# Performance work log

Measured on AMD Instinct MI355X. Metric: run time of the kernel, lower is better.

The kernel has to match this reference:

```python
import jax, jax.numpy as jnp
import numpy as np
import math

D_MODEL = 1024
NUM_HEADS = 16
MAX_LEN = 2048
D_HEAD = D_MODEL // NUM_HEADS
BATCH = 2
SEQ = 2048


def setup_inputs() -> dict:
    root = jax.random.key(0)
    ks = jax.random.split(root, 10)
    s = 1.0 / math.sqrt(D_MODEL)
    return {
        "query": jax.random.normal(ks[0], (BATCH, SEQ, D_MODEL), jnp.float32),
        "key": jax.random.normal(ks[1], (BATCH, SEQ, D_MODEL), jnp.float32),
        "value": jax.random.normal(ks[2], (BATCH, SEQ, D_MODEL), jnp.float32),
        "Wq": jax.random.normal(ks[3], (D_MODEL, D_MODEL), jnp.float32) * s,
        "bq": jax.random.normal(ks[4], (D_MODEL,), jnp.float32) * s,
        "Wk": jax.random.normal(ks[5], (D_MODEL, D_MODEL), jnp.float32) * s,
        "bk": jax.random.normal(ks[6], (D_MODEL,), jnp.float32) * s,
        "Wv": jax.random.normal(ks[7], (D_MODEL, D_MODEL), jnp.float32) * s,
        "bv": jax.random.normal(ks[8], (D_MODEL,), jnp.float32) * s,
        "Er": jax.random.normal(ks[9], (MAX_LEN, D_HEAD), jnp.float32),
    }


def _skew(QEr):
    # QEr: [B, H, S, S] -> pad one zero column on the left, reshape, drop first row
    B, H, R, C = QEr.shape
    padded = jnp.pad(QEr, ((0, 0), (0, 0), (0, 0), (1, 0)))  # [B,H,R,C+1]
    reshaped = padded.reshape(B, H, C + 1, R)
    return reshaped[:, :, 1:, :]  # [B,H,R,C] == Srel


def reference(query, key, value, Wq, bq, Wk, bk, Wv, bv, Er):
    B, S, D = query.shape
    H, dh = NUM_HEADS, D_HEAD
    # nn.Linear: x @ W.T + b
    q = (jnp.einsum("bsd,ed->bse", query, Wq) + bq).reshape(B, S, H, dh).transpose(0, 2, 1, 3)  # [B,H,S,dh]
    k = (jnp.einsum("bsd,ed->bse", key, Wk) + bk).reshape(B, S, H, dh).transpose(0, 2, 1, 3)
    v = (jnp.einsum("bsd,ed->bse", value, Wv) + bv).reshape(B, S, H, dh).transpose(0, 2, 1, 3)
    start = MAX_LEN - S
    Er_s = Er[start:, :]  # [S, dh]
    QEr = jnp.einsum("bhsd,ld->bhsl", q, Er_s)  # [B,H,S,S]
    Srel = _skew(QEr)
    QK = jnp.einsum("bhsd,bhtd->bhst", q, k)
    attn = (QK + Srel) / math.sqrt(dh)
    causal = jnp.tril(jnp.ones((S, S), dtype=bool))
    attn = jnp.where(causal[None, None], attn, -jnp.inf)
    attn = jax.nn.softmax(attn, axis=-1)
    out = jnp.einsum("bhst,bhtd->bhsd", attn, v)  # [B,H,S,dh]
    out = out.transpose(0, 2, 1, 3).reshape(B, S, D)
    return out  # dropout is identity in eval mode
```

## Files before the change

kernel.cpp:

```cpp
#include <hip/hip_runtime.h>
#include <hip/hip_bf16.h>

typedef __attribute__((ext_vector_type(8))) short bf16x8;
typedef __attribute__((ext_vector_type(4))) float f32x4;

#define DEVI __device__ __forceinline__
#define AS1 __attribute__((address_space(1)))
#define AS3 __attribute__((address_space(3)))

constexpr int SEQ_   = 2048;
constexpr int HEADS  = 16;
constexpr int DHEAD  = 64;
constexpr int DMODEL = 1024;

DEVI unsigned short f2bf(float x) {
  __hip_bfloat16 h = __float2bfloat16(x);
  return __builtin_bit_cast(unsigned short, h);
}

DEVI f32x4 MFMA(bf16x8 a, bf16x8 b, f32x4 c) {
  return __builtin_amdgcn_mfma_f32_16x16x32_bf16(a, b, c, 0, 0, 0);
}

DEVI unsigned int cvtpk(float lo, float hi) {
  unsigned int u;
  asm("v_cvt_pk_bf16_f32 %0, %1, %2" : "=v"(u) : "v"(lo), "v"(hi));
  return u;
}

DEVI float exp2v(float x) {
  float y;
  asm("v_exp_f32 %0, %1" : "=v"(y) : "v"(x));
  return y;
}

__global__ void conv_all_kernel(const float* q, const float* k, const float* v,
                                const float* Wq, const float* Wk, const float* Wv,
                                const float* Er,
                                unsigned short* Xq, unsigned short* Xk,
                                unsigned short* Xv,
                                unsigned short* Wqb, unsigned short* Wkb,
                                unsigned short* Wvb, unsigned short* Erb) {
  const int y = blockIdx.y;
  const int i = (blockIdx.x * 256 + threadIdx.x) * 8;
  const float* s;
  unsigned short* d;
  int off = i;
  if (y < 3) {
    if (i >= 2 * SEQ_ * DMODEL) return;
    s = (y == 0) ? q : (y == 1) ? k : v;
    d = (y == 0) ? Xq : (y == 1) ? Xk : Xv;
  } else {
    constexpr int NW = DMODEL * DMODEL;
    if (i >= 3 * NW + SEQ_ * DHEAD) return;
    if (i < NW)          { s = Wq; d = Wqb; }
    else if (i < 2 * NW) { s = Wk; d = Wkb; off = i - NW; }
    else if (i < 3 * NW) { s = Wv; d = Wvb; off = i - 2 * NW; }
    else                 { s = Er; d = Erb; off = i - 3 * NW; }
  }
  const float4* p = (const float4*)(s + off);
  float4 v0 = p[0], v1 = p[1];
  union { unsigned short u[8]; bf16x8 v; } t;
  t.u[0] = f2bf(v0.x); t.u[1] = f2bf(v0.y); t.u[2] = f2bf(v0.z); t.u[3] = f2bf(v0.w);
  t.u[4] = f2bf(v1.x); t.u[5] = f2bf(v1.y); t.u[6] = f2bf(v1.z); t.u[7] = f2bf(v1.w);
  *(bf16x8*)(d + off) = t.v;
}

__global__ __launch_bounds__(256) void proj3_kernel(
    const unsigned short* __restrict__ X0, const unsigned short* __restrict__ X1,
    const unsigned short* __restrict__ X2,
    const unsigned short* __restrict__ W0, const unsigned short* __restrict__ W1,
    const unsigned short* __restrict__ W2,
    const float* __restrict__ bi0, const float* __restrict__ bi1,
    const float* __restrict__ bi2,
    unsigned short* __restrict__ o0, unsigned short* __restrict__ o1,
    unsigned short* __restrict__ o2) {
  const int z = blockIdx.z;
  const unsigned short* X = (z == 0) ? X0 : (z == 1) ? X1 : X2;
  const unsigned short* W = (z == 0) ? W0 : (z == 1) ? W1 : W2;
  const float* bias        = (z == 0) ? bi0 : (z == 1) ? bi1 : bi2;
  unsigned short* out      = (z == 0) ? o0 : (z == 1) ? o1 : o2;

  __shared__ unsigned short Abuf[2][128 * 32];
  __shared__ unsigned short Bbuf[2][128 * 32];
  const int tid  = threadIdx.x;
  const int lane = tid & 63, wv = tid >> 6;
  const int q = lane >> 4, r = lane & 15;
  const int wrow = wv >> 1, wcol = wv & 1;
  const int rowA0 = blockIdx.x * 128, colB0 = blockIdx.y * 128;

  const char* Ag = (const char*)(X + (size_t)rowA0 * DMODEL);
  const char* Bg = (const char*)(W + (size_t)colB0 * DMODEL);

  f32x4 acc[4][4] = {};

  auto stage = [&](int ks, int buf) {
    const int koff = ks * 64;
#pragma unroll
    for (int i = 0; i < 2; ++i) {
      const int b   = (i * 256 + tid) * 16;
      const int row = b >> 6, col = b & 63;
      __builtin_amdgcn_global_load_lds(
          (const AS1 void*)(Ag + (size_t)row * (DMODEL * 2) + koff + col),
          (AS3 void*)((char*)&Abuf[buf][0] + i * 4096 + wv * 1024),
          16, 0, 0);
      __builtin_amdgcn_global_load_lds(
          (const AS1 void*)(Bg + (size_t)row * (DMODEL * 2) + koff + col),
          (AS3 void*)((char*)&Bbuf[buf][0] + i * 4096 + wv * 1024),
          16, 0, 0);
    }
  };

  stage(0, 0);
  for (int ks = 0; ks < 32; ++ks) {
    __syncthreads();
    if (ks + 1 < 32) stage(ks + 1, (ks + 1) & 1);
    const unsigned short* A  = &Abuf[ks & 1][0];
    const unsigned short* Bt = &Bbuf[ks & 1][0];
    bf16x8 af[4], bfr[4];
#pragma unroll
    for (int t = 0; t < 4; ++t) {
      af[t]  = *(const bf16x8*)(A  + (wrow * 64 + t * 16 + r) * 32 + q * 8);
      bfr[t] = *(const bf16x8*)(Bt + (wcol * 64 + t * 16 + r) * 32 + q * 8);
    }
#pragma unroll
    for (int m = 0; m < 4; ++m)
#pragma unroll
      for (int n = 0; n < 4; ++n)
        acc[m][n] = MFMA(af[m], bfr[n], acc[m][n]);
  }

#pragma unroll
  for (int m = 0; m < 4; ++m) {
#pragma unroll
    for (int n = 0; n < 4; ++n) {
      const int e  = colB0 + wcol * 64 + n * 16 + r;
      const float bv = bias[e];
      const int h = e >> 6, dd = e & 63;
      const int nrow0 = rowA0 + wrow * 64 + m * 16 + q * 4;
      const int bb = nrow0 >> 11, ss0 = nrow0 & 2047;
      const size_t bh = (size_t)(bb * HEADS + h);
      if (z == 0) {
#pragma unroll
        for (int j = 0; j < 4; ++j)
          out[(bh * SEQ_ + (ss0 + j)) * DHEAD + dd] =
              f2bf((acc[m][n][j] + bv) * 0.1803368801111244f);
      } else if (z == 1) {
#pragma unroll
        for (int j = 0; j < 4; ++j) {
          const int s = ss0 + j;
          const size_t off = (bh * 64 + (size_t)(s >> 5)) * 2048
                           + (size_t)(((dd >> 5) * 2 + ((s >> 4) & 1)) * 512)
                           + (size_t)(((((dd & 31) >> 3) << 4) + (s & 15)) * 8)
                           + (dd & 7);
          out[off] = f2bf(acc[m][n][j] + bv);
        }
      } else {
#pragma unroll
        for (int j = 0; j < 4; ++j) {
          const int s = ss0 + j;
          const int tile64 = s >> 6, t = s & 63;
          const int tp = 4 * (t & 15) + (t >> 4);
          const int tc = tp >> 5, u = tp & 31;
          const int ln = ((u >> 3) << 4) | (dd & 15);
          const size_t off = (bh * 32 + (size_t)tile64) * 4096
                           + (size_t)(tc * 2048 + (dd >> 4) * 512 + ln * 8 + (u & 7));
          out[off] = f2bf(acc[m][n][j] + bv);
        }
      }
    }
  }
}

struct ErSet { bf16x8 e[8]; };

__global__ __launch_bounds__(256, 2) void attn_kernel(
    const unsigned short* __restrict__ qb, const unsigned short* __restrict__ kt,
    const unsigned short* __restrict__ vt, const unsigned short* __restrict__ Er,
    float* __restrict__ out, float* __restrict__ pO1, float* __restrict__ pL) {
  __shared__ unsigned short k_lds[3][4096];
  __shared__ unsigned short v_lds[3][4096];
  __shared__ unsigned short p_lds[4][32][68];

  const int tid  = threadIdx.x;
  const int lane = tid & 63, wv = tid >> 6;
  const int q = lane >> 4, r = lane & 15;

  const int lid = blockIdx.x;
  const int xcd = lid & 7, idx = lid >> 3;
  const int bh  = (xcd << 2) | (idx & 3);
  const int jb  = idx >> 2;
  const int p = jb >> 1, role = jb & 1;
  const int bb = bh >> 4, hh = bh & 15;

  const unsigned short* qbh = qb + (size_t)bh * SEQ_ * DHEAD;
  const char* ktb = (const char*)(kt + (size_t)bh * 64 * 2048);
  const char* vtb = (const char*)(vt + (size_t)bh * 32 * 4096);
  const f32x4 zero4 = {0.f, 0.f, 0.f, 0.f};

  const char* sgbase = (wv < 2) ? ktb : vtb;
  char* sdst0 = (char*)((wv < 2) ? &k_lds[0][0] : &v_lds[0][0]);
  const int shalf = (wv & 1) * 4096;
  const int soff  = lane * 16;

  auto stageKV = [&](int it, int buf) {
    const char* src = sgbase + (size_t)it * 8192 + shalf + soff;
    char* dst = sdst0 + buf * 8192 + shalf;
#pragma unroll
    for (int c = 0; c < 4; ++c)
      __builtin_amdgcn_global_load_lds((const AS1 void*)(src + c * 1024),
                                       (AS3 void*)(dst + c * 1024), 16, 0, 0);
  };

  auto run_strip = [&](int T, int it0, int it1, float* po, float* pl) {
    const int s0 = T * 128 + wv * 32;
    __syncthreads();
    stageKV(it0, 0);

    bf16x8 qf[2][2];
#pragma unroll
    for (int rt = 0; rt < 2; ++rt) {
      qf[rt][0] = *(const bf16x8*)(qbh + (size_t)(s0 + rt * 16 + r) * DHEAD + q * 8);
      qf[rt][1] = *(const bf16x8*)(qbh + (size_t)(s0 + rt * 16 + r) * DHEAD + 32 + q * 8);
    }

    f32x4 qer[2][6];
    {
      const int lb0 = 2016 + it0 * 64 - s0;
#pragma unroll
      for (int m = 0; m < 2; ++m) {
        int l = lb0 + m * 16 + r; l = l < 2047 ? l : 2047;
        bf16x8 e0 = *(const bf16x8*)(Er + (size_t)l * DHEAD + q * 8);
        bf16x8 e1 = *(const bf16x8*)(Er + (size_t)l * DHEAD + 32 + q * 8);
#pragma unroll
        for (int rt = 0; rt < 2; ++rt)
          qer[rt][m] = MFMA(qf[rt][1], e1, MFMA(qf[rt][0], e0, zero4));
      }
    }

    auto loadE = [&](ErSet& es, int it) {
      const int lb = 2016 + it * 64 - s0;
#pragma unroll
      for (int mi = 0; mi < 4; ++mi) {
        int l = lb + 32 + mi * 16 + r;
        l = l < 2047 ? l : 2047;
        es.e[mi * 2 + 0] = *(const bf16x8*)(Er + (size_t)l * DHEAD + q * 8);
        es.e[mi * 2 + 1] = *(const bf16x8*)(Er + (size_t)l * DHEAD + 32 + q * 8);
      }
    };

    f32x4 oacc[2][4] = {};
    float lpart[2][4] = {};

    auto body = [&](int it, int cur, const ErSet& es) {
      const int t0 = it * 64;
      if (t0 > s0 + 31) return;
      const unsigned short* KL = &k_lds[cur][0];
      const unsigned short* VL = &v_lds[cur][0];

      bf16x8 kf[4][2];
#pragma unroll
      for (int ct = 0; ct < 4; ++ct)
#pragma unroll
        for (int kc = 0; kc < 2; ++kc)
          kf[ct][kc] = *(const bf16x8*)(KL + (ct >> 1) * 2048 + (kc * 2 + (ct & 1)) * 512 + lane * 8);

      f32x4 s4[2][4];
      __builtin_amdgcn_s_setprio(1);
#pragma unroll
      for (int rt = 0; rt < 2; ++rt)
#pragma unroll
        for (int ct = 0; ct < 4; ++ct)
          s4[rt][ct] = MFMA(qf[rt][1], kf[ct][1], MFMA(qf[rt][0], kf[ct][0], zero4));
#pragma unroll
      for (int rt = 0; rt < 2; ++rt)
#pragma unroll
        for (int mi = 0; mi < 4; ++mi)
          qer[rt][2 + mi] = MFMA(qf[rt][1], es.e[mi * 2 + 1],
                                 MFMA(qf[rt][0], es.e[mi * 2 + 0], zero4));
      __builtin_amdgcn_s_setprio(0);

      const int d0 = t0 - s0;
#pragma unroll
      for (int rt = 0; rt < 2; ++rt) {
        const int a = 1 - rt;
#pragma unroll
        for (int j = 0; j < 4; ++j) {
          unsigned int pkA = cvtpk(qer[rt][a][j],     qer[rt][a + 1][j]);
          unsigned int pkB = cvtpk(qer[rt][a + 2][j], qer[rt][a + 3][j]);
          const float  s5f = qer[rt][a + 4][j];
          const int srcl = (q << 4) | ((15 + r - q * 4 - j) & 15);
          unsigned int A = (unsigned int)__shfl((int)pkA, srcl);
          unsigned int B = (unsigned int)__shfl((int)pkB, srcl);
          const float g4 = __shfl(s5f, srcl);
          const float g0 = __builtin_bit_cast(float, A << 16);
          const float g1 = __builtin_bit_cast(float, A & 0xffff0000u);
          const float g2 = __builtin_bit_cast(float, B << 16);
          const float g3 = __builtin_bit_cast(float, B & 0xffff0000u);
          const bool hi = (r > q * 4 + j);
          const float b0 = hi ? g1 : g0;
          const float b1 = hi ? g2 : g1;
          const float b2 = hi ? g3 : g2;
          const float b3 = hi ? g4 : g3;
          const int A_ = rt * 16 + q * 4 + j - r - d0;
          const float p0 = (A_ >= 0)  ? exp2v(s4[rt][0][j] + b0) : 0.f;
          const float p1 = (A_ >= 16) ? exp2v(s4[rt][1][j] + b1) : 0.f;
          const float p2 = (A_ >= 32) ? exp2v(s4[rt][2][j] + b2) : 0.f;
          const float p3 = (A_ >= 48) ? exp2v(s4[rt][3][j] + b3) : 0.f;
          lpart[rt][j] += (p0 + p1) + (p2 + p3);
          const int sl = rt * 16 + q * 4 + j;
          const unsigned long long pw =
              (unsigned long long)cvtpk(p0, p1) |
              ((unsigned long long)cvtpk(p2, p3) << 32);
          *(unsigned long long*)&p_lds[wv][sl][4 * r] = pw;
        }
      }

      bf16x8 vf[4][2];
#pragma unroll
      for (int dc = 0; dc < 4; ++dc)
#pragma unroll
        for (int tc = 0; tc < 2; ++tc)
          vf[dc][tc] = *(const bf16x8*)(VL + tc * 2048 + dc * 512 + lane * 8);
      __builtin_amdgcn_s_setprio(1);
#pragma unroll
      for (int rt = 0; rt < 2; ++rt) {
        bf16x8 pf0 = *(const bf16x8*)(&p_lds[wv][rt * 16 + r][0] + q * 8);
        bf16x8 pf1 = *(const bf16x8*)(&p_lds[wv][rt * 16 + r][0] + 32 + q * 8);
#pragma unroll
        for (int dc = 0; dc < 4; ++dc)
          oacc[rt][dc] = MFMA(pf1, vf[dc][1], MFMA(pf0, vf[dc][0], oacc[rt][dc]));
      }
      __builtin_amdgcn_s_setprio(0);

#pragma unroll
      for (int rt = 0; rt < 2; ++rt) { qer[rt][0] = qer[rt][4]; qer[rt][1] = qer[rt][5]; }
    };

    ErSet eA, eB;
    loadE(eA, it0);

    int it = it0, cur = 0;
    while (true) {
      int nx = cur + 1; if (nx == 3) nx = 0;
      int itn = (it + 1 < it1) ? it + 1 : it1 - 1;
      stageKV(itn, nx);
      loadE(eB, itn);
      asm volatile("s_waitcnt vmcnt(12)\n\ts_barrier" ::: "memory");
      body(it, cur, eA);
      cur = nx;
      if (++it >= it1) break;
      nx = cur + 1; if (nx == 3) nx = 0;
      itn = (it + 1 < it1) ? it + 1 : it1 - 1;
      stageKV(itn, nx);
      loadE(eA, itn);
      asm volatile("s_waitcnt vmcnt(12)\n\ts_barrier" ::: "memory");
      body(it, cur, eB);
      cur = nx;
      if (++it >= it1) break;
    }

#pragma unroll
    for (int rt = 0; rt < 2; ++rt)
#pragma unroll
      for (int j = 0; j < 4; ++j) {
        float ls = lpart[rt][j];
#pragma unroll
        for (int d = 1; d < 16; d <<= 1) ls += __shfl_xor(ls, d);
        const int row = wv * 32 + rt * 16 + q * 4 + j;
        if (po) {
#pragma unroll
          for (int dc = 0; dc < 4; ++dc)
            po[(size_t)row * 64 + dc * 16 + r] = oacc[rt][dc][j];
        } else {
          const int ss = T * 128 + row;
#pragma unroll
          for (int dc = 0; dc < 4; ++dc)
            out[((size_t)(bb * SEQ_ + ss)) * DMODEL + hh * DHEAD + dc * 16 + r] = oacc[rt][dc][j];
        }
        if (r == 0) pl[row] = ls;
      }
  };

  int TA, a1, TB, b0, b1;
  if (role == 0) { TA = 15 - p; a1 = 16 - p; TB = p;      b0 = p + 1;  b1 = 2 * p + 2; }
  else           { TA = p;      a1 = p + 1;  TB = 15 - p; b0 = 16 - p; b1 = 32 - 2 * p; }

  run_strip(TA, 0, a1, nullptr,
            pL + ((size_t)(bh * 16 + TA)) * 256);
  run_strip(TB, b0, b1, pO1 + ((size_t)(bh * 16 + TB)) * 8192,
            pL + ((size_t)(bh * 16 + TB)) * 256 + 128);
}

__global__ __launch_bounds__(256) void reduce_kernel(const float* __restrict__ pO1,
                                                     const float* __restrict__ pL,
                                                     float* __restrict__ out) {
  const int slot = blockIdx.x;
  const int bh = slot >> 4, T = slot & 15;
  const int bb = bh >> 4, hh = bh & 15;
  const int tid = threadIdx.x;
  const int row = tid >> 1, half = (tid & 1) * 32;

  const float l0 = pL[(size_t)slot * 256 + row];
  const float l1 = pL[(size_t)slot * 256 + 128 + row];
  const float inv = 1.0f / (l0 + l1);

  float* a = out + ((size_t)(bb * SEQ_) + T * 128 + row) * DMODEL + hh * DHEAD + half;
  const float* b = pO1 + (size_t)slot * 8192 + row * 64 + half;
#pragma unroll
  for (int k = 0; k < 8; ++k) {
    float4 x = ((const float4*)a)[k];
    float4 y = ((const float4*)b)[k];
    float4 o;
    o.x = (x.x + y.x) * inv; o.y = (x.y + y.y) * inv;
    o.z = (x.z + y.z) * inv; o.w = (x.w + y.w) * inv;
    ((float4*)a)[k] = o;
  }
}

extern "C" void kernel_launch(void* const* d_in, const int* in_sizes, int n_in,
                              void* d_out, int out_size, void* d_ws, size_t ws_size,
                              hipStream_t stream) {
  const float* query = (const float*)d_in[0];
  const float* key   = (const float*)d_in[1];
  const float* value = (const float*)d_in[2];
  const float* Wq    = (const float*)d_in[3];
  const float* bq    = (const float*)d_in[4];
  const float* Wk    = (const float*)d_in[5];
  const float* bk    = (const float*)d_in[6];
  const float* Wv    = (const float*)d_in[7];
  const float* bv    = (const float*)d_in[8];
  const float* Er    = (const float*)d_in[9];

  char* ws = (char*)d_ws;
  unsigned short* qb   = (unsigned short*)(ws + (0u  << 20));
  unsigned short* ktil = (unsigned short*)(ws + (8u  << 20));
  unsigned short* vtil = (unsigned short*)(ws + (16u << 20));
  float*          pO1  = (float*)(ws + (24u << 20));
  float*          pL   = (float*)(ws + (40u << 20));
  unsigned short* Xq   = (unsigned short*)(ws + (32u << 20));
  unsigned short* Xk   = (unsigned short*)(ws + (40u << 20));
  unsigned short* Xv   = (unsigned short*)(ws + (48u << 20));
  unsigned short* Wqb  = (unsigned short*)(ws + (56u << 20));
  unsigned short* Wkb  = (unsigned short*)(ws + (58u << 20));
  unsigned short* Wvb  = (unsigned short*)(ws + (60u << 20));
  unsigned short* Erb  = (unsigned short*)(ws + (62u << 20));

  conv_all_kernel<<<dim3(2048, 4), 256, 0, stream>>>(query, key, value,
                                                     Wq, Wk, Wv, Er,
                                                     Xq, Xk, Xv,
                                                     Wqb, Wkb, Wvb, Erb);

  proj3_kernel<<<dim3(32, 8, 3), 256, 0, stream>>>(Xq, Xk, Xv, Wqb, Wkb, Wvb,
                                                   bq, bk, bv, qb, ktil, vtil);

  attn_kernel<<<dim3(512), 256, 0, stream>>>(qb, ktil, vtil, Erb,
                                             (float*)d_out, pO1, pL);

  reduce_kernel<<<dim3(512), 256, 0, stream>>>(pO1, pL, (float*)d_out);
}
```

Baseline: 140.3 us.

## Split causal attention work into three balanced segments per strip pair with bf16 partials

The attention grid grows from 512 to 768 blocks. Each paired strip set (15-p, p) is split into three KV-range segments so blocks carry more even work, and every segment writes a partial output to workspace. Partials are now stored as bf16, which halves partial traffic, and the reduce kernel sums up to three segment partials per strip. The KV LDS ring drops from triple to double buffering with the barrier moved before the prefetch. This trades extra partial writes and reduce work, plus some precision loss, for better load balance and occupancy.

```diff
diff --git a/kernel.cpp b/kernel.cpp
--- a/kernel.cpp
+++ b/kernel.cpp
@@ -177,9 +177,9 @@
 __global__ __launch_bounds__(256, 2) void attn_kernel(
     const unsigned short* __restrict__ qb, const unsigned short* __restrict__ kt,
     const unsigned short* __restrict__ vt, const unsigned short* __restrict__ Er,
-    float* __restrict__ out, float* __restrict__ pO1, float* __restrict__ pL) {
-  __shared__ unsigned short k_lds[3][4096];
-  __shared__ unsigned short v_lds[3][4096];
+    unsigned short* __restrict__ pO, float* __restrict__ pL) {
+  __shared__ unsigned short k_lds[2][4096];
+  __shared__ unsigned short v_lds[2][4096];
   __shared__ unsigned short p_lds[4][32][68];
 
   const int tid  = threadIdx.x;
@@ -189,9 +189,8 @@
   const int lid = blockIdx.x;
   const int xcd = lid & 7, idx = lid >> 3;
   const int bh  = (xcd << 2) | (idx & 3);
-  const int jb  = idx >> 2;
-  const int p = jb >> 1, role = jb & 1;
-  const int bb = bh >> 4, hh = bh & 15;
+  const int rest = idx >> 2;
+  const int p = rest / 3, seg = rest - p * 3;
 
   const unsigned short* qbh = qb + (size_t)bh * SEQ_ * DHEAD;
   const char* ktb = (const char*)(kt + (size_t)bh * 64 * 2048);
@@ -212,7 +211,7 @@
                                        (AS3 void*)(dst + c * 1024), 16, 0, 0);
   };
 
-  auto run_strip = [&](int T, int it0, int it1, float* po, float* pl) {
+  auto run_strip = [&](int T, int it0, int it1, unsigned short* po, float* pl) {
     const int s0 = T * 128 + wv * 32;
     __syncthreads();
     stageKV(it0, 0);
@@ -230,6 +229,7 @@
 #pragma unroll
       for (int m = 0; m < 2; ++m) {
         int l = lb0 + m * 16 + r; l = l < 2047 ? l : 2047;
+        l = l < 0 ? 0 : l;
         bf16x8 e0 = *(const bf16x8*)(Er + (size_t)l * DHEAD + q * 8);
         bf16x8 e1 = *(const bf16x8*)(Er + (size_t)l * DHEAD + 32 + q * 8);
 #pragma unroll
@@ -342,21 +342,23 @@
 
     int it = it0, cur = 0;
     while (true) {
-      int nx = cur + 1; if (nx == 3) nx = 0;
-      int itn = (it + 1 < it1) ? it + 1 : it1 - 1;
-      stageKV(itn, nx);
-      loadE(eB, itn);
-      asm volatile("s_waitcnt vmcnt(12)\n\ts_barrier" ::: "memory");
+      asm volatile("s_waitcnt vmcnt(8)\n\ts_barrier" ::: "memory");
+      {
+        const int itn = (it + 1 < it1) ? it + 1 : it1 - 1;
+        stageKV(itn, cur ^ 1);
+        loadE(eB, itn);
+      }
       body(it, cur, eA);
-      cur = nx;
+      cur ^= 1;
       if (++it >= it1) break;
-      nx = cur + 1; if (nx == 3) nx = 0;
-      itn = (it + 1 < it1) ? it + 1 : it1 - 1;
-      stageKV(itn, nx);
-      loadE(eA, itn);
-      asm volatile("s_waitcnt vmcnt(12)\n\ts_barrier" ::: "memory");
+      asm volatile("s_waitcnt vmcnt(8)\n\ts_barrier" ::: "memory");
+      {
+        const int itn = (it + 1 < it1) ? it + 1 : it1 - 1;
+        stageKV(itn, cur ^ 1);
+        loadE(eA, itn);
+      }
       body(it, cur, eB);
-      cur = nx;
+      cur ^= 1;
       if (++it >= it1) break;
     }
 
@@ -368,31 +370,31 @@
 #pragma unroll
         for (int d = 1; d < 16; d <<= 1) ls += __shfl_xor(ls, d);
         const int row = wv * 32 + rt * 16 + q * 4 + j;
-        if (po) {
-#pragma unroll
-          for (int dc = 0; dc < 4; ++dc)
-            po[(size_t)row * 64 + dc * 16 + r] = oacc[rt][dc][j];
-        } else {
-          const int ss = T * 128 + row;
-#pragma unroll
-          for (int dc = 0; dc < 4; ++dc)
-            out[((size_t)(bb * SEQ_ + ss)) * DMODEL + hh * DHEAD + dc * 16 + r] = oacc[rt][dc][j];
-        }
+#pragma unroll
+        for (int dc = 0; dc < 4; ++dc)
+          po[(size_t)row * 64 + dc * 16 + r] = f2bf(oacc[rt][dc][j]);
         if (r == 0) pl[row] = ls;
       }
   };
 
-  int TA, a1, TB, b0, b1;
-  if (role == 0) { TA = 15 - p; a1 = 16 - p; TB = p;      b0 = p + 1;  b1 = 2 * p + 2; }
-  else           { TA = p;      a1 = p + 1;  TB = 15 - p; b0 = 16 - p; b1 = 32 - 2 * p; }
-
-  run_strip(TA, 0, a1, nullptr,
-            pL + ((size_t)(bh * 16 + TA)) * 256);
-  run_strip(TB, b0, b1, pO1 + ((size_t)(bh * 16 + TB)) * 8192,
-            pL + ((size_t)(bh * 16 + TB)) * 256 + 128);
-}
-
-__global__ __launch_bounds__(256) void reduce_kernel(const float* __restrict__ pO1,
+  const int a  = (seg == 0) ? 0 : (seg == 1) ? 12 : 23;
+  const int b  = (seg == 0) ? 12 : (seg == 1) ? 23 : 34;
+  const int LA = 32 - 2 * p;
+  const int TAt = 15 - p, TBt = p;
+
+  if (a < LA) {
+    const size_t slot = ((size_t)(bh * 16 + TAt)) * 3 + seg;
+    const int e = (b < LA) ? b : LA;
+    run_strip(TAt, a, e, pO + slot * 8192, pL + slot * 128);
+  }
+  if (b > LA) {
+    const size_t slot = ((size_t)(bh * 16 + TBt)) * 3 + seg;
+    const int s = (a > LA) ? a - LA : 0;
+    run_strip(TBt, s, b - LA, pO + slot * 8192, pL + slot * 128);
+  }
+}
+
+__global__ __launch_bounds__(256) void reduce_kernel(const unsigned short* __restrict__ pO,
                                                      const float* __restrict__ pL,
                                                      float* __restrict__ out) {
   const int slot = blockIdx.x;
@@ -401,20 +403,33 @@
   const int tid = threadIdx.x;
   const int row = tid >> 1, half = (tid & 1) * 32;
 
-  const float l0 = pL[(size_t)slot * 256 + row];
-  const float l1 = pL[(size_t)slot * 256 + 128 + row];
-  const float inv = 1.0f / (l0 + l1);
-
-  float* a = out + ((size_t)(bb * SEQ_) + T * 128 + row) * DMODEL + hh * DHEAD + half;
-  const float* b = pO1 + (size_t)slot * 8192 + row * 64 + half;
-#pragma unroll
-  for (int k = 0; k < 8; ++k) {
-    float4 x = ((const float4*)a)[k];
-    float4 y = ((const float4*)b)[k];
+  const int s_lo = (T >= 8) ? 0 : (T >= 5) ? 1 : 2;
+  const int s_hi = (T >= 11) ? 3 : (T >= 8) ? 2 : 3;
+
+  float l = 0.f;
+  float acc[32] = {};
+  for (int s = s_lo; s < s_hi; ++s) {
+    const size_t sb = (size_t)slot * 3 + s;
+    l += pL[sb * 128 + row];
+    const unsigned short* src = pO + sb * 8192 + row * 64 + half;
+#pragma unroll
+    for (int c = 0; c < 4; ++c) {
+      union { bf16x8 v; unsigned short u[8]; } w;
+      w.v = *(const bf16x8*)(src + c * 8);
+#pragma unroll
+      for (int e = 0; e < 8; ++e)
+        acc[c * 8 + e] += __builtin_bit_cast(float, (unsigned int)w.u[e] << 16);
+    }
+  }
+
+  const float inv = 1.0f / l;
+  float* dst = out + ((size_t)(bb * SEQ_) + T * 128 + row) * DMODEL + hh * DHEAD + half;
+#pragma unroll
+  for (int c = 0; c < 8; ++c) {
     float4 o;
-    o.x = (x.x + y.x) * inv; o.y = (x.y + y.y) * inv;
-    o.z = (x.z + y.z) * inv; o.w = (x.w + y.w) * inv;
-    ((float4*)a)[k] = o;
+    o.x = acc[c * 4 + 0] * inv; o.y = acc[c * 4 + 1] * inv;
+    o.z = acc[c * 4 + 2] * inv; o.w = acc[c * 4 + 3] * inv;
+    ((float4*)dst)[c] = o;
   }
 }
 
@@ -436,8 +451,8 @@
   unsigned short* qb   = (unsigned short*)(ws + (0u  << 20));
   unsigned short* ktil = (unsigned short*)(ws + (8u  << 20));
   unsigned short* vtil = (unsigned short*)(ws + (16u << 20));
-  float*          pO1  = (float*)(ws + (24u << 20));
-  float*          pL   = (float*)(ws + (40u << 20));
+  unsigned short* pO   = (unsigned short*)(ws + (24u << 20));
+  float*          pL   = (float*)(ws + (50u << 20));
   unsigned short* Xq   = (unsigned short*)(ws + (32u << 20));
   unsigned short* Xk   = (unsigned short*)(ws + (40u << 20));
   unsigned short* Xv   = (unsigned short*)(ws + (48u << 20));
@@ -454,8 +469,7 @@
   proj3_kernel<<<dim3(32, 8, 3), 256, 0, stream>>>(Xq, Xk, Xv, Wqb, Wkb, Wvb,
                                                    bq, bk, bv, qb, ktil, vtil);
 
-  attn_kernel<<<dim3(512), 256, 0, stream>>>(qb, ktil, vtil, Erb,
-                                             (float*)d_out, pO1, pL);
-
-  reduce_kernel<<<dim3(512), 256, 0, stream>>>(pO1, pL, (float*)d_out);
-}
+  attn_kernel<<<dim3(768), 256, 0, stream>>>(qb, ktil, vtil, Erb, pO, pL);
+
+  reduce_kernel<<<dim3(512), 256, 0, stream>>>(pO, pL, (float*)d_out);
+}
```

Result: slower. 154.3 us (+10.0%).
